# Performance work log

Measured on AMD Instinct MI355X. Metric: run time of the kernel, lower is better.

The kernel has to match this reference:

```python
import jax, jax.numpy as jnp
import numpy as np

K = 64        # num_clusters
S1 = 5        # num_shadow + 1
C = 128       # dim
ALPHA = 1500.0
EPS = 1e-12


def setup_inputs() -> dict:
    key = jax.random.key(0)
    k1, k2 = jax.random.split(key)
    x = jax.random.normal(k1, (8, C, 44, 44), dtype=jnp.float32)
    centroids = jax.random.normal(k2, (K, S1, C), dtype=jnp.float32) * 0.01
    return {"x": x, "centroids": centroids}


def reference(x, centroids):
    N = x.shape[0]
    # conv params derived from centroids, as in _init_params
    w = (2.0 * ALPHA) * centroids.reshape(K * S1, C)            # (K*S1, C)
    b = -ALPHA * jnp.linalg.norm(centroids.reshape(K * S1, C), axis=1)  # (K*S1,)

    xf = x.reshape(N, C, -1)                                    # (N, C, P)
    # 1x1 conv == GEMM over channel dim
    logits = jnp.einsum('mc,ncp->nmp', w, xf) + b[None, :, None]
    logits = logits.reshape(N, K, S1, -1)                       # (N, K, S1, P)

    soft_alpha = jax.nn.softmax(logits[:, :, 0:1, :], axis=1)   # (N, K, 1, P)
    soft_beta = jax.nn.softmax(logits, axis=2)[:, :, 0:1, :]    # (N, K, 1, P)
    soft_assign = soft_alpha * soft_beta                        # (N, K, 1, P)

    # residual = x - rep_centroid; then residual *= (1 + soft_assign); sum over P.
    # sum_p (x[n,c,p] - rep[k,c]) * w[n,k,p]
    #   = einsum(w, x) - rep[k,c] * sum_p w[n,k,p]   (same math, no (N,K,C,P) tensor)
    w_assign = 1.0 + soft_assign[:, :, 0, :]                    # (N, K, P)
    rep = centroids[:, 0, :]                                    # (K, C)
    out = jnp.einsum('nkp,ncp->nkc', w_assign, xf) \
          - rep[None, :, :] * jnp.sum(w_assign, axis=-1)[:, :, None]  # (N, K, C)

    # intra-cluster L2 normalize (dim=2), flatten, global L2 normalize
    out = out / jnp.maximum(jnp.linalg.norm(out, axis=2, keepdims=True), EPS)
    flat = out.reshape(N, -1)
    flat = flat / jnp.maximum(jnp.linalg.norm(flat, axis=1, keepdims=True), EPS)
    return (flat, soft_assign)
```

## Files before the change

kernel.cpp:

```cpp
#include <hip/hip_runtime.h>
#include <math.h>

#define NB 8
#define KC 64
#define S1C 5
#define CC 128
#define PP 1936
#define MM 320
#define PT 64
#define NPT 31
#define NTILE (NB * NPT)
#define ALPHAF 1500.0f
#define EPSF 1e-12f

#define WS_CENPK 65536
#define WS_GBIAS 512
#define WS_HDR   (WS_CENPK + WS_GBIAS)
#define WS_PART  ((size_t)NTILE * KC * CC)
#define WS_MAIN_FLOATS (WS_HDR + WS_PART + (size_t)NTILE * KC)

typedef __attribute__((ext_vector_type(8))) short short8;
typedef __attribute__((ext_vector_type(4))) float f32x4;

__device__ __forceinline__ unsigned pack_bf16s(float x) {
    unsigned u  = __float_as_uint(x);
    unsigned hi = u & 0xffff0000u;
    float lo    = x - __uint_as_float(hi);
    return hi | (__float_as_uint(lo) >> 16);
}

__device__ __forceinline__ void unpack8(const int4 q0, const int4 q1,
                                        short8& h, short8& l) {
    const int d[8] = {q0.x, q0.y, q0.z, q0.w, q1.x, q1.y, q1.z, q1.w};
#pragma unroll
    for (int j = 0; j < 8; ++j) {
        h[j] = (short)((unsigned)d[j] >> 16);
        l[j] = (short)((unsigned)d[j] & 0xffffu);
    }
}

__device__ __forceinline__ void split8(const float4 a, const float4 b,
                                       short8& h, short8& l) {
    const float f[8] = {a.x, a.y, a.z, a.w, b.x, b.y, b.z, b.w};
#pragma unroll
    for (int j = 0; j < 8; ++j) {
        const unsigned u  = __float_as_uint(f[j]);
        const unsigned hi = u & 0xffff0000u;
        const float lo    = f[j] - __uint_as_float(hi);
        h[j] = (short)(hi >> 16);
        l[j] = (short)(__float_as_uint(lo) >> 16);
    }
}

__global__ __launch_bounds__(64) void k0_pack(
    const float* __restrict__ cen, unsigned* __restrict__ cenPk,
    float* __restrict__ gbias)
{
    const int nt   = blockIdx.x;
    const int l    = threadIdx.x;
    const int l15  = l & 15;
    const int quad = l >> 4;
    const int mp   = nt * 16 + l15;
    const int s    = mp & 7;
    const bool valid = (s < 5);
    const int wrow = 5 * (mp >> 3) + s;
    short8* dst8 = (short8*)cenPk;
    float ss = 0.f;
#pragma unroll
    for (int ks = 0; ks < 4; ++ks) {
        float4 v0 = make_float4(0.f, 0.f, 0.f, 0.f), v1 = v0;
        if (valid) {
            const float* wp = cen + (size_t)wrow * CC + ks * 32 + quad * 8;
            v0 = *(const float4*)wp;
            v1 = *(const float4*)(wp + 4);
        }
        ss += v0.x * v0.x + v0.y * v0.y + v0.z * v0.z + v0.w * v0.w
            + v1.x * v1.x + v1.y * v1.y + v1.z * v1.z + v1.w * v1.w;
        short8 h, lo;
        split8(v0, v1, h, lo);
        const int base = ((ks * 32 + nt) * 64 + l) * 2;
        dst8[base]     = h;
        dst8[base + 1] = lo;
    }
    ss += __shfl_xor(ss, 16);
    ss += __shfl_xor(ss, 32);
    if (quad == 0) gbias[mp] = valid ? (-ALPHAF * sqrtf(ss)) : -3.0e38f;
}

__global__ __launch_bounds__(1024, 4) void k1_main(
    const float* __restrict__ x, const unsigned* __restrict__ cenPk,
    const float* __restrict__ gbias,
    float* __restrict__ sa_out, float* __restrict__ outC,
    float* __restrict__ outS, int mode)
{
    __shared__ unsigned xbuf[CC * 68];
    __shared__ unsigned war[KC * 68];
    __shared__ float2   ap[16 * 66];
    __shared__ float    bias_p[512];

    const int tid  = threadIdx.x;
    const int lane = tid & 63;
    const int wid  = tid >> 6;
    const int quad = lane >> 4;
    const int l15  = lane & 15;
    const int bx   = blockIdx.x;
    const int n    = bx / NPT;
    const int pt   = bx - n * NPT;
    const int p0   = pt * PT;

    const float* xn = x + (size_t)n * CC * PP;
    for (int idx = tid; idx < CC * 16; idx += 1024) {
        const int c = idx >> 4;
        const int q = idx & 15;
        const int p = 4 * q;
        float4 v = make_float4(0.f, 0.f, 0.f, 0.f);
        if (p0 + p < PP) v = *(const float4*)(xn + (size_t)c * PP + p0 + p);
        xbuf[(p + 0) * 132 + c] = pack_bf16s(v.x);
        xbuf[(p + 1) * 132 + c] = pack_bf16s(v.y);
        xbuf[(p + 2) * 132 + c] = pack_bf16s(v.z);
        xbuf[(p + 3) * 132 + c] = pack_bf16s(v.w);
    }
    if (tid < 512) bias_p[tid] = gbias[tid];
    __syncthreads();

    f32x4 dacc[4][2];
#pragma unroll
    for (int a = 0; a < 4; ++a) {
        dacc[a][0] = (f32x4){0.f, 0.f, 0.f, 0.f};
        dacc[a][1] = (f32x4){0.f, 0.f, 0.f, 0.f};
    }
    const short8* cpk8 = (const short8*)cenPk;

#pragma unroll 1
    for (int ks = 0; ks < 4; ++ks) {
        short8 bh[2], bl[2];
#pragma unroll
        for (int i = 0; i < 2; ++i) {
            const int boff = ((ks * 32 + 2 * wid + i) * 64 + lane) * 2;
            bh[i] = cpk8[boff];
            bl[i] = cpk8[boff + 1];
        }
#pragma unroll
        for (int a = 0; a < 4; ++a) {
            const int abase = (a * 16 + l15) * 132 + ks * 32 + quad * 8;
            const int4 q0 = *(const int4*)(&xbuf[abase]);
            const int4 q1 = *(const int4*)(&xbuf[abase + 4]);
            short8 ah, al;
            unpack8(q0, q1, ah, al);
#pragma unroll
            for (int i = 0; i < 2; ++i) {
                dacc[a][i] = __builtin_amdgcn_mfma_f32_16x16x32_bf16(ah, bh[i], dacc[a][i], 0, 0, 0);
                dacc[a][i] = __builtin_amdgcn_mfma_f32_16x16x32_bf16(ah, bl[i], dacc[a][i], 0, 0, 0);
                dacc[a][i] = __builtin_amdgcn_mfma_f32_16x16x32_bf16(al, bh[i], dacc[a][i], 0, 0, 0);
            }
        }
    }

    const float bv0 = bias_p[(2 * wid + 0) * 16 + l15];
    const float bv1 = bias_p[(2 * wid + 1) * 16 + l15];
#pragma unroll
    for (int a = 0; a < 4; ++a)
#pragma unroll
        for (int r = 0; r < 4; ++r) {
            dacc[a][0][r] = 2.f * ALPHAF * dacc[a][0][r] + bv0;
            dacc[a][1][r] = 2.f * ALPHAF * dacc[a][1][r] + bv1;
        }

#pragma unroll
    for (int a = 0; a < 4; ++a) {
        f32x4 mx4, se4;
#pragma unroll
        for (int r = 0; r < 4; ++r) {
            float m_ = fmaxf(dacc[a][0][r], dacc[a][1][r]);
            m_ = fmaxf(m_, __shfl_xor(m_, 8));
            float se = __expf(dacc[a][0][r] - m_) + __expf(dacc[a][1][r] - m_);
            se += __shfl_xor(se, 8);
            mx4[r] = m_; se4[r] = se;
        }
        if (l15 == 0) {
#pragma unroll
            for (int r = 0; r < 4; ++r)
                ap[wid * 66 + a * 16 + 4 * quad + r] = make_float2(mx4[r], se4[r]);
        }
    }
    __syncthreads();

    float gmv, arv;
    {
        float gm = -3.0e38f;
#pragma unroll
        for (int w = 0; w < 16; ++w) gm = fmaxf(gm, ap[w * 66 + lane].x);
        float s = 0.f;
#pragma unroll
        for (int w = 0; w < 16; ++w) {
            const float2 v = ap[w * 66 + lane];
            s += v.y * __expf(v.x - gm);
        }
        gmv = gm; arv = 1.0f / s;
    }

    float* san = sa_out + (size_t)n * KC * PP;
    float psum[2] = {0.f, 0.f};
    const bool is_s0 = ((l15 & 7) == 0);
#pragma unroll
    for (int a = 0; a < 4; ++a) {
#pragma unroll
        for (int i = 0; i < 2; ++i) {
            const f32x4 lg = dacc[a][i];
            f32x4 sav; unsigned wpk[4];
#pragma unroll
            for (int r = 0; r < 4; ++r) {
                float m_ = lg[r];
                m_ = fmaxf(m_, __shfl_xor(m_, 1));
                m_ = fmaxf(m_, __shfl_xor(m_, 2));
                m_ = fmaxf(m_, __shfl_xor(m_, 4));
                const float e_ = __expf(lg[r] - m_);
                float d_ = e_;
                d_ += __shfl_xor(d_, 1);
                d_ += __shfl_xor(d_, 2);
                d_ += __shfl_xor(d_, 4);
                const int p = a * 16 + 4 * quad + r;
                const float gm_p = __shfl(gmv, p);
                const float ar_p = __shfl(arv, p);
                const float sa = __expf(lg[r] - gm_p) * ar_p * (e_ / d_);
                const bool pvalid = (p0 + p) < PP;
                const float wa = pvalid ? (1.0f + sa) : 0.0f;
                sav[r] = sa;
                wpk[r] = pack_bf16s(wa);
                psum[i] += wa;
            }
            const int k = 4 * wid + 2 * i + (l15 >> 3);
            if (is_s0) {
                *(int4*)(&war[k * 68 + a * 16 + 4 * quad]) = *(const int4*)wpk;
                const int pg = p0 + a * 16 + 4 * quad;
                if (pg < PP) *(float4*)(&san[(size_t)k * PP + pg]) = *(const float4*)&sav;
            }
        }
    }
#pragma unroll
    for (int i = 0; i < 2; ++i) {
        float s = psum[i];
        s += __shfl_xor(s, 16);
        s += __shfl_xor(s, 32);
        if (is_s0 && quad == 0) {
            const int k = 4 * wid + 2 * i + (l15 >> 3);
            if (mode == 0) outS[(size_t)bx * KC + k] = s;
            else           atomicAdd(&outS[(size_t)n * KC + k], s);
        }
    }
    {
        const int c  = tid >> 3;
        const int po = (tid & 7) * 8;
        float4 v0 = make_float4(0.f, 0.f, 0.f, 0.f), v1 = v0;
        if (p0 + po < PP) {
            const float* src = xn + (size_t)c * PP + p0 + po;
            v0 = *(const float4*)src;
            v1 = *(const float4*)(src + 4);
        }
        unsigned pk[8];
        pk[0] = pack_bf16s(v0.x); pk[1] = pack_bf16s(v0.y);
        pk[2] = pack_bf16s(v0.z); pk[3] = pack_bf16s(v0.w);
        pk[4] = pack_bf16s(v1.x); pk[5] = pack_bf16s(v1.y);
        pk[6] = pack_bf16s(v1.z); pk[7] = pack_bf16s(v1.w);
        *(int4*)(&xbuf[c * 68 + po])     = *(const int4*)&pk[0];
        *(int4*)(&xbuf[c * 68 + po + 4]) = *(const int4*)&pk[4];
    }
    __syncthreads();

    const int kt  = wid & 3;
    const int ct0 = (wid >> 2) * 2;
    f32x4 cacc[2];
    cacc[0] = (f32x4){0.f, 0.f, 0.f, 0.f};
    cacc[1] = (f32x4){0.f, 0.f, 0.f, 0.f};
#pragma unroll
    for (int ks = 0; ks < 64; ks += 32) {
        const int abase = (kt * 16 + l15) * 68 + ks + quad * 8;
        const int4 qa0 = *(const int4*)(&war[abase]);
        const int4 qa1 = *(const int4*)(&war[abase + 4]);
        short8 ah, al;
        unpack8(qa0, qa1, ah, al);
#pragma unroll
        for (int t = 0; t < 2; ++t) {
            const int c = (ct0 + t) * 16 + l15;
            const int bbase = c * 68 + ks + quad * 8;
            const int4 qb0 = *(const int4*)(&xbuf[bbase]);
            const int4 qb1 = *(const int4*)(&xbuf[bbase + 4]);
            short8 bh, bl;
            unpack8(qb0, qb1, bh, bl);
            cacc[t] = __builtin_amdgcn_mfma_f32_16x16x32_bf16(ah, bh, cacc[t], 0, 0, 0);
            cacc[t] = __builtin_amdgcn_mfma_f32_16x16x32_bf16(ah, bl, cacc[t], 0, 0, 0);
            cacc[t] = __builtin_amdgcn_mfma_f32_16x16x32_bf16(al, bh, cacc[t], 0, 0, 0);
        }
    }
    if (mode == 0) {
        float* dst = outC + (size_t)bx * KC * CC;
#pragma unroll
        for (int t = 0; t < 2; ++t) {
            const int c = (ct0 + t) * 16 + l15;
#pragma unroll
            for (int r = 0; r < 4; ++r)
                dst[(kt * 16 + 4 * quad + r) * CC + c] = cacc[t][r];
        }
    } else {
        float* dst = outC + (size_t)n * KC * CC;
#pragma unroll
        for (int t = 0; t < 2; ++t) {
            const int c = (ct0 + t) * 16 + l15;
#pragma unroll
            for (int r = 0; r < 4; ++r)
                atomicAdd(&dst[(kt * 16 + 4 * quad + r) * CC + c], cacc[t][r]);
        }
    }
}

__global__ __launch_bounds__(128) void k2_slab(
    const float* __restrict__ part, const float* __restrict__ ps,
    const float* __restrict__ cen, float* __restrict__ flat)
{
    __shared__ float w2[2];
    const int b = blockIdx.x;
    const int n = b >> 6;
    const int k = b & 63;
    const int c = threadIdx.x;
    const float* pb = part + (size_t)n * NPT * KC * CC + (size_t)k * CC + c;
    float v = 0.f;
#pragma unroll 8
    for (int pt = 0; pt < NPT; ++pt) v += pb[(size_t)pt * KC * CC];
    const float* psb = ps + (size_t)n * NPT * KC + k;
    float sw = 0.f;
#pragma unroll
    for (int pt = 0; pt < NPT; ++pt) sw += psb[(size_t)pt * KC];
    v -= cen[(size_t)k * S1C * CC + c] * sw;

    float ss = v * v;
#pragma unroll
    for (int off = 32; off > 0; off >>= 1) ss += __shfl_down(ss, off);
    if ((c & 63) == 0) w2[c >> 6] = ss;
    __syncthreads();
    const float norm = sqrtf(w2[0] + w2[1]);
    const float scale = 1.0f / (fmaxf(norm, EPSF) * 8.0f);
    flat[(size_t)b * CC + c] = v * scale;
}

__global__ __launch_bounds__(128) void k2_final(
    const float* __restrict__ accC, const float* __restrict__ accS,
    const float* __restrict__ cen, float* __restrict__ flat)
{
    __shared__ float w2[2];
    const int b = blockIdx.x;
    const int k = b & 63;
    const int c = threadIdx.x;
    const float v = accC[(size_t)b * CC + c] -
                    cen[(size_t)k * S1C * CC + c] * accS[b];
    float ss = v * v;
#pragma unroll
    for (int off = 32; off > 0; off >>= 1) ss += __shfl_down(ss, off);
    if ((c & 63) == 0) w2[c >> 6] = ss;
    __syncthreads();
    const float norm = sqrtf(w2[0] + w2[1]);
    const float scale = 1.0f / (fmaxf(norm, EPSF) * 8.0f);
    flat[(size_t)b * CC + c] = v * scale;
}

extern "C" void kernel_launch(void* const* d_in, const int* in_sizes, int n_in,
                              void* d_out, int out_size, void* d_ws, size_t ws_size,
                              hipStream_t stream) {
    const float* x   = (const float*)d_in[0];
    const float* cen = (const float*)d_in[1];
    float* out  = (float*)d_out;
    float* flat = out;
    float* sa   = out + (size_t)NB * KC * CC;
    float* ws   = (float*)d_ws;

    unsigned* cenPk = (unsigned*)ws;
    float*    gbias = ws + WS_CENPK;

    if (ws_size >= WS_MAIN_FLOATS * 4) {
        float* part = ws + WS_HDR;
        float* ps   = part + WS_PART;
        k0_pack<<<32, 64, 0, stream>>>(cen, cenPk, gbias);
        k1_main<<<NTILE, 1024, 0, stream>>>(x, cenPk, gbias, sa, part, ps, 0);
        k2_slab<<<NB * KC, 128, 0, stream>>>(part, ps, cen, flat);
    } else {
        float* accC = ws + WS_HDR;
        float* accS = accC + (size_t)NB * KC * CC;
        hipMemsetAsync(accC, 0, (size_t)(NB * KC * CC + NB * KC) * 4, stream);
        k0_pack<<<32, 64, 0, stream>>>(cen, cenPk, gbias);
        k1_main<<<NTILE, 1024, 0, stream>>>(x, cenPk, gbias, sa, accC, accS, 1);
        k2_final<<<NB * KC, 128, 0, stream>>>(accC, accS, cen, flat);
    }
}
```

Measured before the change: 90.92 us.

## Load x once into registers, prefetch first centroid slice, defer soft_assign stores

Each thread now loads its x tile once into registers before the first GEMM and reuses those packed values for the second GEMM's layout, so x is no longer read from global memory twice. Bias and the first k-slice of packed centroids are read straight into registers at kernel start instead of going through shared memory. The soft_assign output is no longer written with scattered float4 stores inside the softmax loop. It is written at the end as coalesced rows reconstructed from the bf16 hi/lo weights held in shared memory. The cost is eight extra registers held across the first phase, and soft_assign is rebuilt from a split-bf16 approximation of 1+sa, which may lose some precision.

```diff
diff --git a/kernel.cpp b/kernel.cpp
--- a/kernel.cpp
+++ b/kernel.cpp
@@ -96,7 +96,6 @@
     __shared__ unsigned xbuf[CC * 68];
     __shared__ unsigned war[KC * 68];
     __shared__ float2   ap[16 * 66];
-    __shared__ float    bias_p[512];
 
     const int tid  = threadIdx.x;
     const int lane = tid & 63;
@@ -108,19 +107,35 @@
     const int pt   = bx - n * NPT;
     const int p0   = pt * PT;
 
+    const float bv0 = gbias[(2 * wid + 0) * 16 + l15];
+    const float bv1 = gbias[(2 * wid + 1) * 16 + l15];
+    const short8* cpk8 = (const short8*)cenPk;
+    short8 bh0[2], bl0[2];
+#pragma unroll
+    for (int i = 0; i < 2; ++i) {
+        const int boff = ((2 * wid + i) * 64 + lane) * 2;
+        bh0[i] = cpk8[boff];
+        bl0[i] = cpk8[boff + 1];
+    }
+
     const float* xn = x + (size_t)n * CC * PP;
-    for (int idx = tid; idx < CC * 16; idx += 1024) {
-        const int c = idx >> 4;
-        const int q = idx & 15;
-        const int p = 4 * q;
-        float4 v = make_float4(0.f, 0.f, 0.f, 0.f);
-        if (p0 + p < PP) v = *(const float4*)(xn + (size_t)c * PP + p0 + p);
-        xbuf[(p + 0) * 132 + c] = pack_bf16s(v.x);
-        xbuf[(p + 1) * 132 + c] = pack_bf16s(v.y);
-        xbuf[(p + 2) * 132 + c] = pack_bf16s(v.z);
-        xbuf[(p + 3) * 132 + c] = pack_bf16s(v.w);
-    }
-    if (tid < 512) bias_p[tid] = gbias[tid];
+    const int sc  = tid >> 3;
+    const int spo = (tid & 7) * 8;
+    unsigned pk[8];
+    {
+        float4 v0 = make_float4(0.f, 0.f, 0.f, 0.f), v1 = v0;
+        if (p0 + spo < PP) {
+            const float* src = xn + (size_t)sc * PP + p0 + spo;
+            v0 = *(const float4*)src;
+            v1 = *(const float4*)(src + 4);
+        }
+        pk[0] = pack_bf16s(v0.x); pk[1] = pack_bf16s(v0.y);
+        pk[2] = pack_bf16s(v0.z); pk[3] = pack_bf16s(v0.w);
+        pk[4] = pack_bf16s(v1.x); pk[5] = pack_bf16s(v1.y);
+        pk[6] = pack_bf16s(v1.z); pk[7] = pack_bf16s(v1.w);
+#pragma unroll
+        for (int j = 0; j < 8; ++j) xbuf[(spo + j) * 132 + sc] = pk[j];
+    }
     __syncthreads();
 
     f32x4 dacc[4][2];
@@ -129,20 +144,11 @@
         dacc[a][0] = (f32x4){0.f, 0.f, 0.f, 0.f};
         dacc[a][1] = (f32x4){0.f, 0.f, 0.f, 0.f};
     }
-    const short8* cpk8 = (const short8*)cenPk;
-
-#pragma unroll 1
-    for (int ks = 0; ks < 4; ++ks) {
-        short8 bh[2], bl[2];
-#pragma unroll
-        for (int i = 0; i < 2; ++i) {
-            const int boff = ((ks * 32 + 2 * wid + i) * 64 + lane) * 2;
-            bh[i] = cpk8[boff];
-            bl[i] = cpk8[boff + 1];
-        }
+
+    auto mfma_step = [&](const int ksoff, const short8 bh[2], const short8 bl[2]) {
 #pragma unroll
         for (int a = 0; a < 4; ++a) {
-            const int abase = (a * 16 + l15) * 132 + ks * 32 + quad * 8;
+            const int abase = (a * 16 + l15) * 132 + ksoff + quad * 8;
             const int4 q0 = *(const int4*)(&xbuf[abase]);
             const int4 q1 = *(const int4*)(&xbuf[abase + 4]);
             short8 ah, al;
@@ -154,10 +160,21 @@
                 dacc[a][i] = __builtin_amdgcn_mfma_f32_16x16x32_bf16(al, bh[i], dacc[a][i], 0, 0, 0);
             }
         }
-    }
-
-    const float bv0 = bias_p[(2 * wid + 0) * 16 + l15];
-    const float bv1 = bias_p[(2 * wid + 1) * 16 + l15];
+    };
+
+    mfma_step(0, bh0, bl0);
+#pragma unroll 1
+    for (int ks = 1; ks < 4; ++ks) {
+        short8 bh[2], bl[2];
+#pragma unroll
+        for (int i = 0; i < 2; ++i) {
+            const int boff = ((ks * 32 + 2 * wid + i) * 64 + lane) * 2;
+            bh[i] = cpk8[boff];
+            bl[i] = cpk8[boff + 1];
+        }
+        mfma_step(ks * 32, bh, bl);
+    }
+
 #pragma unroll
     for (int a = 0; a < 4; ++a)
 #pragma unroll
@@ -185,6 +202,9 @@
     }
     __syncthreads();
 
+    *(int4*)(&xbuf[sc * 68 + spo])     = *(const int4*)&pk[0];
+    *(int4*)(&xbuf[sc * 68 + spo + 4]) = *(const int4*)&pk[4];
+
     float gmv, arv;
     {
         float gm = -3.0e38f;
@@ -199,7 +219,6 @@
         gmv = gm; arv = 1.0f / s;
     }
 
-    float* san = sa_out + (size_t)n * KC * PP;
     float psum[2] = {0.f, 0.f};
     const bool is_s0 = ((l15 & 7) == 0);
 #pragma unroll
@@ -207,7 +226,7 @@
 #pragma unroll
         for (int i = 0; i < 2; ++i) {
             const f32x4 lg = dacc[a][i];
-            f32x4 sav; unsigned wpk[4];
+            unsigned wpk[4];
 #pragma unroll
             for (int r = 0; r < 4; ++r) {
                 float m_ = lg[r];
@@ -225,16 +244,12 @@
                 const float sa = __expf(lg[r] - gm_p) * ar_p * (e_ / d_);
                 const bool pvalid = (p0 + p) < PP;
                 const float wa = pvalid ? (1.0f + sa) : 0.0f;
-                sav[r] = sa;
                 wpk[r] = pack_bf16s(wa);
                 psum[i] += wa;
             }
             const int k = 4 * wid + 2 * i + (l15 >> 3);
-            if (is_s0) {
+            if (is_s0)
                 *(int4*)(&war[k * 68 + a * 16 + 4 * quad]) = *(const int4*)wpk;
-                const int pg = p0 + a * 16 + 4 * quad;
-                if (pg < PP) *(float4*)(&san[(size_t)k * PP + pg]) = *(const float4*)&sav;
-            }
         }
     }
 #pragma unroll
@@ -247,23 +262,6 @@
             if (mode == 0) outS[(size_t)bx * KC + k] = s;
             else           atomicAdd(&outS[(size_t)n * KC + k], s);
         }
-    }
-    {
-        const int c  = tid >> 3;
-        const int po = (tid & 7) * 8;
-        float4 v0 = make_float4(0.f, 0.f, 0.f, 0.f), v1 = v0;
-        if (p0 + po < PP) {
-            const float* src = xn + (size_t)c * PP + p0 + po;
-            v0 = *(const float4*)src;
-            v1 = *(const float4*)(src + 4);
-        }
-        unsigned pk[8];
-        pk[0] = pack_bf16s(v0.x); pk[1] = pack_bf16s(v0.y);
-        pk[2] = pack_bf16s(v0.z); pk[3] = pack_bf16s(v0.w);
-        pk[4] = pack_bf16s(v1.x); pk[5] = pack_bf16s(v1.y);
-        pk[6] = pack_bf16s(v1.z); pk[7] = pack_bf16s(v1.w);
-        *(int4*)(&xbuf[c * 68 + po])     = *(const int4*)&pk[0];
-        *(int4*)(&xbuf[c * 68 + po + 4]) = *(const int4*)&pk[4];
     }
     __syncthreads();
 
@@ -309,6 +307,27 @@
 #pragma unroll
             for (int r = 0; r < 4; ++r)
                 atomicAdd(&dst[(kt * 16 + 4 * quad + r) * CC + c], cacc[t][r]);
+        }
+    }
+
+    {
+        float* san = sa_out + (size_t)n * KC * PP;
+        const int k  = tid >> 4;
+        const int p4 = (tid & 15) * 4;
+        const int pg = p0 + p4;
+        if (pg < PP) {
+            const int4 q = *(const int4*)(&war[k * 68 + p4]);
+            const int d[4] = {q.x, q.y, q.z, q.w};
+            float4 sv;
+            float* svp = &sv.x;
+#pragma unroll
+            for (int j = 0; j < 4; ++j) {
+                const unsigned u = (unsigned)d[j];
+                const float wa = __uint_as_float(u & 0xffff0000u)
+                               + __uint_as_float(u << 16);
+                svp[j] = wa - 1.0f;
+            }
+            *(float4*)(&san[(size_t)k * PP + pg]) = sv;
         }
     }
 }
```

Result: no change. 91.14 us (+0.2%).
